# Optimization experiments

Measured on AMD Instinct MI355X. Metric: run time of the kernel, lower is better.

The kernel has to match this reference:

```python
import jax, jax.numpy as jnp
import numpy as np

HEADS = 8
DIM_HEAD = 64  # note: per-head dim is inner_dim/heads = 512 due to the module's inner_dim = dim_head*dim
SCALE = DIM_HEAD ** (-0.5)
EPS = 1e-5


def layernorm(x, gamma):
    # nn.LayerNorm(dim, elementwise_affine=False) then x * (gamma + 1)
    mu = jnp.mean(x, axis=-1, keepdims=True)
    var = jnp.var(x, axis=-1, keepdims=True)
    xn = (x - mu) * jax.lax.rsqrt(var + EPS)
    return xn * (gamma + 1.0)


def setup_inputs() -> dict:
    key = jax.random.key(0)
    ks = jax.random.split(key, 6)
    b, n, dim = 2, 2048, 256
    inner = DIM_HEAD * dim  # 4096
    x = jax.random.normal(ks[0], (b, n, dim), dtype=jnp.float32)
    gamma = jax.random.normal(ks[1], (dim,), dtype=jnp.float32) * 0.02
    Wq = jax.random.normal(ks[2], (inner, dim), dtype=jnp.float32) * 0.02
    Wk = jax.random.normal(ks[3], (inner, dim), dtype=jnp.float32) * 0.02
    Wv = jax.random.normal(ks[4], (inner, dim), dtype=jnp.float32) * 0.02
    Wo = jax.random.normal(ks[5], (dim, inner), dtype=jnp.float32) * 0.02
    return {"x": x, "gamma": gamma, "Wq": Wq, "Wk": Wk, "Wv": Wv, "Wo": Wo}


def reference(x, gamma, Wq, Wk, Wv, Wo):
    b, n, dim = x.shape
    h = HEADS
    xn = layernorm(x, gamma)  # reuse_attention=True -> norm = LayerNorm(dim)
    # self-attention: context = xn (cross_attend=False, norm_context=Identity)
    q = jnp.einsum('bnd,ed->bne', xn, Wq).reshape(b, n, h, -1).transpose(0, 2, 1, 3)
    k = jnp.einsum('bnd,ed->bne', xn, Wk).reshape(b, n, h, -1).transpose(0, 2, 1, 3)
    v = jnp.einsum('bnd,ed->bne', xn, Wv).reshape(b, n, h, -1).transpose(0, 2, 1, 3)
    qk_sim = jnp.einsum('bhqd,bhkd->bhqk', q * SCALE, k)
    attn = jax.nn.softmax(qk_sim, axis=-1)  # dropout p=0.0 -> identity
    dot = jnp.einsum('bhqk,bhkd->bhqd', attn, v)
    out = dot.transpose(0, 2, 1, 3).reshape(b, n, -1)
    out = jnp.einsum('bne,de->bnd', out, Wo)
    return out
```

## Files before the change

### kernel.cpp

```cpp
#include <hip/hip_runtime.h>


typedef unsigned short u16;
typedef unsigned int u32;
typedef __bf16 bf16x8 __attribute__((ext_vector_type(8)));
typedef float f32x4 __attribute__((ext_vector_type(4)));

__device__ __forceinline__ u16 f2bf(float f) {
    u32 u = __builtin_bit_cast(u32, f);
    u += 0x7fffu + ((u >> 16) & 1u);
    return (u16)(u >> 16);
}

#define GLDS16(G, L)                                                                  \
    __builtin_amdgcn_global_load_lds((const __attribute__((address_space(1))) u32*)(G), \
                                     (__attribute__((address_space(3))) u32*)(L), 16, 0, 0)

template <int N> __device__ __forceinline__ void vm_wait() {
    asm volatile("s_waitcnt vmcnt(%0)" :: "n"(N) : "memory");
}
__device__ __forceinline__ void lgk0() {
    asm volatile("s_waitcnt lgkmcnt(0)" ::: "memory");
}
__device__ __forceinline__ void bar() {
    __builtin_amdgcn_s_barrier();
    __builtin_amdgcn_sched_barrier(0);
}

template <typename OutT, bool ATOMIC>
__device__ __forceinline__ void gemm_core(
    const u16* __restrict__ A, const u16* __restrict__ B, OutT* __restrict__ C,
    int K, int lda, int ldb, int ldc)
{
    __shared__ u16 ldsA[3][128 * 32];
    __shared__ u16 ldsB[3][128 * 32];

    const int bm = blockIdx.y * 128;
    const int bn = blockIdx.x * 128;
    const int t = threadIdx.x;
    const int w = t >> 6, l = t & 63;
    const int wm = w >> 1, wn = w & 1;
    const int lr = l & 15, lk = l >> 4;
    const int sw = lk ^ ((lr >> 1) & 3);

    const int m0 = t >> 2, s0 = t & 3;
    const int c0 = s0 ^ ((m0 >> 1) & 3);
    const int m1 = 64 + m0;
    const int c1 = s0 ^ ((m1 >> 1) & 3);
    const int o0 = (t & ~63) * 8;
    const int o1 = (256 + (t & ~63)) * 8;

    const u16* gA0 = A + (size_t)(bm + m0) * lda + c0 * 8;
    const u16* gA1 = A + (size_t)(bm + m1) * lda + c1 * 8;
    const u16* gB0 = B + (size_t)(bn + m0) * ldb + c0 * 8;
    const u16* gB1 = B + (size_t)(bn + m1) * ldb + c1 * 8;

    f32x4 acc[4][4];
#pragma unroll
    for (int i = 0; i < 4; ++i)
#pragma unroll
        for (int j = 0; j < 4; ++j)
            acc[i][j] = f32x4{0.f, 0.f, 0.f, 0.f};

    const int nk = K >> 5;

    GLDS16(gA0, &ldsA[0][o0]); GLDS16(gA1, &ldsA[0][o1]);
    GLDS16(gB0, &ldsB[0][o0]); GLDS16(gB1, &ldsB[0][o1]);
    gA0 += 32; gA1 += 32; gB0 += 32; gB1 += 32;
    GLDS16(gA0, &ldsA[1][o0]); GLDS16(gA1, &ldsA[1][o1]);
    GLDS16(gB0, &ldsB[1][o0]); GLDS16(gB1, &ldsB[1][o1]);
    gA0 += 32; gA1 += 32; gB0 += 32; gB1 += 32;

    int cur = 0, wsl = 2;
    for (int kt = 0; kt < nk - 1; ++kt) {
        vm_wait<4>(); bar();
        if (kt + 2 < nk) {
            GLDS16(gA0, &ldsA[wsl][o0]); GLDS16(gA1, &ldsA[wsl][o1]);
            GLDS16(gB0, &ldsB[wsl][o0]); GLDS16(gB1, &ldsB[wsl][o1]);
            gA0 += 32; gA1 += 32; gB0 += 32; gB1 += 32;
        }
        bf16x8 av[4], bv[4];
#pragma unroll
        for (int i = 0; i < 4; ++i) {
            av[i] = *(const bf16x8*)&ldsA[cur][(wm * 64 + i * 16 + lr) * 32 + sw * 8];
            bv[i] = *(const bf16x8*)&ldsB[cur][(wn * 64 + i * 16 + lr) * 32 + sw * 8];
        }
        __builtin_amdgcn_s_setprio(1);
#pragma unroll
        for (int i = 0; i < 4; ++i)
#pragma unroll
            for (int j = 0; j < 4; ++j)
                acc[i][j] = __builtin_amdgcn_mfma_f32_16x16x32_bf16(av[i], bv[j], acc[i][j], 0, 0, 0);
        __builtin_amdgcn_s_setprio(0);
        cur = (cur == 2) ? 0 : cur + 1;
        wsl = (wsl == 2) ? 0 : wsl + 1;
    }
    vm_wait<0>(); bar();
    {
        bf16x8 av[4], bv[4];
#pragma unroll
        for (int i = 0; i < 4; ++i) {
            av[i] = *(const bf16x8*)&ldsA[cur][(wm * 64 + i * 16 + lr) * 32 + sw * 8];
            bv[i] = *(const bf16x8*)&ldsB[cur][(wn * 64 + i * 16 + lr) * 32 + sw * 8];
        }
        __builtin_amdgcn_s_setprio(1);
#pragma unroll
        for (int i = 0; i < 4; ++i)
#pragma unroll
            for (int j = 0; j < 4; ++j)
                acc[i][j] = __builtin_amdgcn_mfma_f32_16x16x32_bf16(av[i], bv[j], acc[i][j], 0, 0, 0);
        __builtin_amdgcn_s_setprio(0);
    }

#pragma unroll
    for (int i = 0; i < 4; ++i) {
        const int row0 = bm + wm * 64 + i * 16 + lk * 4;
#pragma unroll
        for (int j = 0; j < 4; ++j) {
            const int col = bn + wn * 64 + j * 16 + lr;
#pragma unroll
            for (int r = 0; r < 4; ++r) {
                const size_t idx = (size_t)(row0 + r) * ldc + col;
                const float v = acc[i][j][r];
                if constexpr (ATOMIC) {
                    atomicAdd(&C[idx], v);
                } else if constexpr (sizeof(OutT) == 2) {
                    C[idx] = (OutT)f2bf(v);
                } else {
                    C[idx] = (OutT)v;
                }
            }
        }
    }
}

__global__ void __launch_bounds__(256, 3) gemm_w(
    const u16* __restrict__ wkt, const u16* __restrict__ wqt,
    const u16* __restrict__ wo, const u16* __restrict__ wvt,
    float* __restrict__ MtF)
{
    const int z = blockIdx.z;
    const int zh = z & 7;
    const int q = z >> 3;
    const int which = q & 1;
    const int kc = q >> 1;
    const u16* A; const u16* B; float* C; int lda;
    if (which == 0) {
        A = wkt + (size_t)zh * 524288 + kc * 512; lda = 2048;
        B = wqt + (size_t)zh * 524288 + kc * 512;
        C = MtF + (size_t)zh * 65536;
    } else {
        A = wo + (size_t)zh * 2048 + kc * 512;    lda = 16384;
        B = wvt + (size_t)zh * 524288 + kc * 512;
        C = MtF + 524288 + (size_t)zh * 65536;
    }
    gemm_core<float, true>(A, B, C, 512, lda, 2048, 256);
}

__global__ void __launch_bounds__(256, 3) gemm_yz(
    const u16* __restrict__ xn, const u16* __restrict__ Mt,
    const u16* __restrict__ Nb, u16* __restrict__ Y, u16* __restrict__ Zt)
{
    const int z = blockIdx.z;
    const u16* A; const u16* B; u16* C;
    if (z < 2) {
        A = xn + (size_t)z * 524288;
        B = Mt;
        C = Y + (size_t)z * 4194304;
    } else {
        const int b = z - 2;
        A = Nb;
        B = xn + (size_t)b * 524288;
        C = Zt + (size_t)b * 4194304;
    }
    gemm_core<u16, false>(A, B, C, 256, 256, 256, 2048);
}

__global__ void __launch_bounds__(256) prep_kernel(
    const float* __restrict__ x, const float* __restrict__ g,
    const float* __restrict__ Wq, const float* __restrict__ Wk,
    const float* __restrict__ Wv, const float* __restrict__ Wo,
    u16* __restrict__ wqkv, u16* __restrict__ wo_b,
    u16* __restrict__ xn, float* __restrict__ MtF)
{
    __shared__ u16 tile[64][66];
    const int bid = blockIdx.x;
    const int t = threadIdx.x;
    if (bid < 3072) {
        const int bx = bid & 31, by = (bid >> 5) & 3, z = bid >> 7;
        const int wsel = z >> 3, h = z & 7;
        const float* src = (wsel == 0) ? Wq : (wsel == 1) ? Wk : Wv;
        const float scale = (wsel == 0) ? 0.125f : 1.0f;
        u16* d = wqkv + (size_t)wsel * 4194304;
        const int d0 = bx * 64;
        const int a0 = by * 64;
        const int c = t & 63, r0 = t >> 6;
#pragma unroll
        for (int rr = 0; rr < 16; ++rr) {
            const int r = r0 + rr * 4;
            tile[r][c] = f2bf(src[((size_t)h * 2048 + d0 + r) * 256 + a0 + c] * scale);
        }
        __syncthreads();
#pragma unroll
        for (int rr = 0; rr < 16; ++rr) {
            const int r = r0 + rr * 4;
            d[((size_t)h * 256 + a0 + r) * 2048 + d0 + c] = tile[c][r];
        }
    } else if (bid < 7168) {
        const size_t i = (size_t)(bid - 3072) * 256 + t;
        const float4 v = ((const float4*)Wo)[i];
        ushort4 o4;
        o4.x = f2bf(v.x); o4.y = f2bf(v.y); o4.z = f2bf(v.z); o4.w = f2bf(v.w);
        ((ushort4*)wo_b)[i] = o4;
    } else if (bid < 8192) {
        const size_t row = (size_t)(bid - 7168) * 4 + (t >> 6);
        const int l = t & 63;
        const float4 v = ((const float4*)(x + row * 256))[l];
        float s = v.x + v.y + v.z + v.w;
        float qq = v.x * v.x + v.y * v.y + v.z * v.z + v.w * v.w;
#pragma unroll
        for (int o = 32; o > 0; o >>= 1) {
            s += __shfl_xor(s, o, 64);
            qq += __shfl_xor(qq, o, 64);
        }
        const float mu = s * (1.0f / 256.0f);
        const float var = qq * (1.0f / 256.0f) - mu * mu;
        const float rs = rsqrtf(var + 1e-5f);
        const float4 gg = ((const float4*)g)[l];
        ushort4 o4;
        o4.x = f2bf((v.x - mu) * rs * (gg.x + 1.0f));
        o4.y = f2bf((v.y - mu) * rs * (gg.y + 1.0f));
        o4.z = f2bf((v.z - mu) * rs * (gg.z + 1.0f));
        o4.w = f2bf((v.w - mu) * rs * (gg.w + 1.0f));
        ((ushort4*)(xn + row * 256))[l] = o4;
    } else {
        const size_t i = (size_t)(bid - 8192) * 256 + t;
        ((float4*)MtF)[i] = float4{0.f, 0.f, 0.f, 0.f};
    }
}

__global__ void __launch_bounds__(256, 2) attn_fused(
    const u16* __restrict__ Y, const u16* __restrict__ xn,
    const u16* __restrict__ Zt, float* __restrict__ opart)
{
    __shared__ u16 ldsB[3][128 * 32];
    __shared__ u16 ldsZ[2][256 * 32];
    __shared__ u16 Pl[64 * 136];
    __shared__ float l_lds[64];

    const int wgid = blockIdx.x + 32 * blockIdx.y;
    const int xcd = wgid & 7;
    const int p = wgid >> 3;
    const int hb = 2 * xcd + (p & 1);
    const int i0 = (p >> 1) * 64;
    const int h = hb >> 1, b = hb & 1;

    const int t = threadIdx.x;
    const int w = t >> 6, l = t & 63;
    const int wm = w >> 1, wn = w & 1;
    const int lr = l & 15, lk = l >> 4;
    const int sw = lk ^ ((lr >> 1) & 3);

    if (t < 64) l_lds[t] = 0.f;

    const u16* Yb = Y + (size_t)(b * 2048 + i0) * 2048 + h * 256;
    const u16* xb = xn + (size_t)b * 2048 * 256;
    const u16* Zb = Zt + (size_t)b * 4194304 + (size_t)h * 524288;

    const int m0 = t >> 2, s0 = t & 3;
    const int c0 = s0 ^ ((m0 >> 1) & 3);
    const int m1 = 64 + m0;
    const int c1 = s0 ^ ((m1 >> 1) & 3);
    const int oB0 = (t & ~63) * 8;
    const int oB1 = (256 + (t & ~63)) * 8;

    const u16 *gZ0, *gZ1, *gZ2, *gZ3;
    const int oZ0 = (t & ~63) * 8;
    const int oZ1 = (256 + (t & ~63)) * 8;
    const int oZ2 = (512 + (t & ~63)) * 8;
    const int oZ3 = (768 + (t & ~63)) * 8;
    {
        const int q0 = t, q1 = 256 + t, q2 = 512 + t, q3 = 768 + t;
        const int mz0 = q0 >> 2, mz1 = q1 >> 2, mz2 = q2 >> 2, mz3 = q3 >> 2;
        const int cz0 = (q0 & 3) ^ ((mz0 >> 1) & 3);
        const int cz1 = (q1 & 3) ^ ((mz1 >> 1) & 3);
        const int cz2 = (q2 & 3) ^ ((mz2 >> 1) & 3);
        const int cz3 = (q3 & 3) ^ ((mz3 >> 1) & 3);
        gZ0 = Zb + (size_t)mz0 * 2048 + cz0 * 8;
        gZ1 = Zb + (size_t)mz1 * 2048 + cz1 * 8;
        gZ2 = Zb + (size_t)mz2 * 2048 + cz2 * 8;
        gZ3 = Zb + (size_t)mz3 * 2048 + cz3 * 8;
    }

    u16* ldsY = &ldsZ[0][0];
#pragma unroll
    for (int pp = 0; pp < 8; ++pp) {
        const int q = pp * 256 + t;
        const int kt = q >> 8, qq = q & 255;
        const int m = qq >> 2, s = qq & 3;
        const int c = s ^ ((m >> 1) & 3);
        GLDS16(Yb + (size_t)m * 2048 + kt * 32 + c * 8,
               &ldsY[(pp * 256 + (t & ~63)) * 8]);
    }
    GLDS16(xb + (size_t)m0 * 256 + c0 * 8, &ldsB[0][oB0]);
    GLDS16(xb + (size_t)m1 * 256 + c1 * 8, &ldsB[0][oB1]);
    GLDS16(xb + (size_t)m0 * 256 + 32 + c0 * 8, &ldsB[1][oB0]);
    GLDS16(xb + (size_t)m1 * 256 + 32 + c1 * 8, &ldsB[1][oB1]);
    vm_wait<4>();
    bar();

    bf16x8 yr[8][2];
#pragma unroll
    for (int kt = 0; kt < 8; ++kt)
#pragma unroll
        for (int i = 0; i < 2; ++i)
            yr[kt][i] = *(const bf16x8*)&ldsY[kt * 2048 + (wm * 32 + i * 16 + lr) * 32 + sw * 8];

    f32x4 acc_o[2][8];
#pragma unroll
    for (int i = 0; i < 2; ++i)
#pragma unroll
        for (int j = 0; j < 8; ++j)
            acc_o[i][j] = f32x4{0.f, 0.f, 0.f, 0.f};
    float lsum[8];
#pragma unroll
    for (int i = 0; i < 8; ++i) lsum[i] = 0.f;

#define S_STEP(KT, VMC, ISSUE)                                                        \
    {                                                                                 \
        vm_wait<VMC>(); bar();                                                        \
        ISSUE;                                                                        \
        bf16x8 bv[4];                                                                 \
        _Pragma("unroll")                                                             \
        for (int j = 0; j < 4; ++j)                                                   \
            bv[j] = *(const bf16x8*)&ldsB[(KT) % 3][(wn * 64 + j * 16 + lr) * 32 + sw * 8]; \
        __builtin_amdgcn_s_setprio(1);                                                \
        _Pragma("unroll")                                                             \
        for (int j = 0; j < 4; ++j) {                                                 \
            acc_s[0][j] = __builtin_amdgcn_mfma_f32_16x16x32_bf16(yr[KT][0], bv[j], acc_s[0][j], 0, 0, 0); \
            acc_s[1][j] = __builtin_amdgcn_mfma_f32_16x16x32_bf16(yr[KT][1], bv[j], acc_s[1][j], 0, 0, 0); \
        }                                                                             \
        __builtin_amdgcn_s_setprio(0);                                                \
    }

#define PV_STEP(KT, VMC, ISSUE)                                                       \
    {                                                                                 \
        vm_wait<VMC>(); bar();                                                        \
        ISSUE;                                                                        \
        bf16x8 av[2];                                                                 \
        av[0] = *(const bf16x8*)&Pl[(wm * 32 + lr) * 136 + (KT) * 32 + lk * 8];       \
        av[1] = *(const bf16x8*)&Pl[(wm * 32 + 16 + lr) * 136 + (KT) * 32 + lk * 8];  \
        __builtin_amdgcn_s_setprio(1);                                                \
        _Pragma("unroll")                                                             \
        for (int jf = 0; jf < 8; ++jf) {                                              \
            const bf16x8 bz = *(const bf16x8*)&ldsZ[(KT) & 1][(wn * 128 + jf * 16 + lr) * 32 + sw * 8]; \
            acc_o[0][jf] = __builtin_amdgcn_mfma_f32_16x16x32_bf16(av[0], bz, acc_o[0][jf], 0, 0, 0);   \
            acc_o[1][jf] = __builtin_amdgcn_mfma_f32_16x16x32_bf16(av[1], bz, acc_o[1][jf], 0, 0, 0);   \
        }                                                                             \
        __builtin_amdgcn_s_setprio(0);                                                \
    }

#define ISSUE_B(JBASE, KK, SLOT)                                                      \
    GLDS16(JBASE + (size_t)m0 * 256 + (KK) * 32 + c0 * 8, &ldsB[SLOT][oB0]);          \
    GLDS16(JBASE + (size_t)m1 * 256 + (KK) * 32 + c1 * 8, &ldsB[SLOT][oB1])

#define ISSUE_Z(OFF, ZBUF)                                                            \
    GLDS16(gZ0 + (OFF), &ldsZ[ZBUF][oZ0]);                                            \
    GLDS16(gZ1 + (OFF), &ldsZ[ZBUF][oZ1]);                                            \
    GLDS16(gZ2 + (OFF), &ldsZ[ZBUF][oZ2]);                                            \
    GLDS16(gZ3 + (OFF), &ldsZ[ZBUF][oZ3])

    for (int jt = 0; jt < 16; ++jt) {
        const int j0 = jt * 128;
        const int jn = ((jt + 1) & 15) * 128;
        const u16* xbj = xb + (size_t)j0 * 256;
        const u16* xbn = xb + (size_t)jn * 256;

        f32x4 acc_s[2][4];
#pragma unroll
        for (int i = 0; i < 2; ++i)
#pragma unroll
            for (int j = 0; j < 4; ++j)
                acc_s[i][j] = f32x4{0.f, 0.f, 0.f, 0.f};

        S_STEP(0, 2, ISSUE_B(xbj, 2, 2))
        S_STEP(1, 2, ISSUE_B(xbj, 3, 0))
        S_STEP(2, 2, ISSUE_B(xbj, 4, 1))
        S_STEP(3, 2, ISSUE_B(xbj, 5, 2))
        S_STEP(4, 2, ISSUE_B(xbj, 6, 0))
        S_STEP(5, 2, ISSUE_B(xbj, 7, 1))
        S_STEP(6, 2, ISSUE_Z(j0, 0))
        S_STEP(7, 4, ISSUE_Z(j0 + 32, 1))

#pragma unroll
        for (int i = 0; i < 2; ++i)
#pragma unroll
            for (int j = 0; j < 4; ++j)
#pragma unroll
                for (int r = 0; r < 4; ++r) {
                    const float e = __expf(acc_s[i][j][r]);
                    lsum[i * 4 + r] += e;
                    Pl[(wm * 32 + i * 16 + lk * 4 + r) * 136 + wn * 64 + j * 16 + lr] = f2bf(e);
                }
        lgk0();

        PV_STEP(0, 4, ((void)0))
        PV_STEP(1, 0, ISSUE_Z(j0 + 64, 0))
        PV_STEP(2, 0, ISSUE_Z(j0 + 96, 1); ISSUE_B(xbn, 0, 0))
        PV_STEP(3, 2, ISSUE_B(xbn, 1, 1))
    }

#pragma unroll
    for (int i = 0; i < 2; ++i)
#pragma unroll
        for (int r = 0; r < 4; ++r) {
            float s = lsum[i * 4 + r];
            s += __shfl_xor(s, 1, 64);
            s += __shfl_xor(s, 2, 64);
            s += __shfl_xor(s, 4, 64);
            s += __shfl_xor(s, 8, 64);
            if (lr == 0) atomicAdd(&l_lds[wm * 32 + i * 16 + lk * 4 + r], s);
        }
    __syncthreads();

    float* oh = opart + (size_t)h * 1048576;
#pragma unroll
    for (int i = 0; i < 2; ++i)
#pragma unroll
        for (int r = 0; r < 4; ++r) {
            const int row = wm * 32 + i * 16 + lk * 4 + r;
            const float rl = 1.0f / l_lds[row];
            float* orow = oh + (size_t)(b * 2048 + i0 + row) * 256 + wn * 128;
#pragma unroll
            for (int jf = 0; jf < 8; ++jf)
                orow[jf * 16 + lr] = acc_o[i][jf][r] * rl;
        }
}

__global__ void __launch_bounds__(256) hreduce_kernel(const float* __restrict__ opart,
                                                      float* __restrict__ out)
{
    const size_t i = (size_t)blockIdx.x * 256 + threadIdx.x;
    float4 s = ((const float4*)opart)[i];
#pragma unroll
    for (int h = 1; h < 8; ++h) {
        const float4 v = ((const float4*)(opart + (size_t)h * 1048576))[i];
        s.x += v.x; s.y += v.y; s.z += v.z; s.w += v.w;
    }
    ((float4*)out)[i] = s;
}

__global__ void __launch_bounds__(256) cast_bf16_kernel(const float* __restrict__ src,
                                                        u16* __restrict__ dst, float scale)
{
    const size_t i = (size_t)blockIdx.x * 256 + threadIdx.x;
    const float4 v = ((const float4*)src)[i];
    ushort4 o4;
    o4.x = f2bf(v.x * scale);
    o4.y = f2bf(v.y * scale);
    o4.z = f2bf(v.z * scale);
    o4.w = f2bf(v.w * scale);
    ((ushort4*)dst)[i] = o4;
}

extern "C" void kernel_launch(void* const* d_in, const int* in_sizes, int n_in,
                              void* d_out, int out_size, void* d_ws, size_t ws_size,
                              hipStream_t stream)
{
    (void)in_sizes; (void)n_in; (void)ws_size; (void)out_size;
    const float* x     = (const float*)d_in[0];
    const float* gamma = (const float*)d_in[1];
    const float* Wq    = (const float*)d_in[2];
    const float* Wk    = (const float*)d_in[3];
    const float* Wv    = (const float*)d_in[4];
    const float* Wo    = (const float*)d_in[5];
    float* out = (float*)d_out;

    char* ws = (char*)d_ws;
    const size_t MB = 1048576;
    u16* wqt   = (u16*)(ws);
    u16* wkt   = (u16*)(ws + 8 * MB);
    u16* wvt   = (u16*)(ws + 16 * MB);
    u16* wo    = (u16*)(ws + 24 * MB);
    u16* xn    = (u16*)(ws + 32 * MB);
    u16* Mt    = (u16*)(ws + 34 * MB);
    float* MtF = (float*)(ws + 36 * MB);
    u16* Nb    = (u16*)(ws + 35 * MB);
    u16* Y     = (u16*)(ws + 44 * MB);
    u16* Zt    = (u16*)(ws + 60 * MB);
    float* opart = (float*)(ws);

    prep_kernel<<<9216, 256, 0, stream>>>(x, gamma, Wq, Wk, Wv, Wo, wqt, wo, xn, MtF);

    gemm_w<<<dim3(2, 2, 64), 256, 0, stream>>>(wkt, wqt, wo, wvt, MtF);

    cast_bf16_kernel<<<1024, 256, 0, stream>>>(MtF, Mt, 1.0f);

    gemm_yz<<<dim3(16, 16, 4), 256, 0, stream>>>(xn, Mt, Nb, Y, Zt);

    attn_fused<<<dim3(32, 16), 256, 0, stream>>>(Y, xn, Zt, opart);

    hreduce_kernel<<<1024, 256, 0, stream>>>(opart, out);
}
```

Measured before the change: 253.8 us.

## Drop split-K atomics in weight GEMM and write bf16 output directly

The weight-product GEMM no longer splits K into four chunks with fp32 atomic accumulation. Each block now runs the full K=2048 reduction and writes bf16 results directly. This removes the MtF zeroing in prep, the atomics, and the separate cast kernel, saving two launches' worth of traffic. In exchange the grid shrinks from 256 to 64 blocks, each doing four times the work, so fewer CUs are kept busy.

```diff
diff --git a/kernel.cpp b/kernel.cpp
--- a/kernel.cpp
+++ b/kernel.cpp
@@ -137,24 +137,22 @@
 __global__ void __launch_bounds__(256, 3) gemm_w(
     const u16* __restrict__ wkt, const u16* __restrict__ wqt,
     const u16* __restrict__ wo, const u16* __restrict__ wvt,
-    float* __restrict__ MtF)
+    u16* __restrict__ Mt)
 {
     const int z = blockIdx.z;
-    const int zh = z & 7;
-    const int q = z >> 3;
-    const int which = q & 1;
-    const int kc = q >> 1;
-    const u16* A; const u16* B; float* C; int lda;
+    const int zh = z >> 1;
+    const int which = z & 1;
+    const u16* A; const u16* B; u16* C; int lda;
     if (which == 0) {
-        A = wkt + (size_t)zh * 524288 + kc * 512; lda = 2048;
-        B = wqt + (size_t)zh * 524288 + kc * 512;
-        C = MtF + (size_t)zh * 65536;
+        A = wkt + (size_t)zh * 524288; lda = 2048;
+        B = wqt + (size_t)zh * 524288;
+        C = Mt + (size_t)zh * 65536;
     } else {
-        A = wo + (size_t)zh * 2048 + kc * 512;    lda = 16384;
-        B = wvt + (size_t)zh * 524288 + kc * 512;
-        C = MtF + 524288 + (size_t)zh * 65536;
-    }
-    gemm_core<float, true>(A, B, C, 512, lda, 2048, 256);
+        A = wo + (size_t)zh * 2048;    lda = 16384;
+        B = wvt + (size_t)zh * 524288;
+        C = Mt + 524288 + (size_t)zh * 65536;
+    }
+    gemm_core<u16, false>(A, B, C, 2048, lda, 2048, 256);
 }
 
 __global__ void __launch_bounds__(256, 3) gemm_yz(
@@ -181,7 +179,7 @@
     const float* __restrict__ Wq, const float* __restrict__ Wk,
     const float* __restrict__ Wv, const float* __restrict__ Wo,
     u16* __restrict__ wqkv, u16* __restrict__ wo_b,
-    u16* __restrict__ xn, float* __restrict__ MtF)
+    u16* __restrict__ xn)
 {
     __shared__ u16 tile[64][66];
     const int bid = blockIdx.x;
@@ -212,7 +210,7 @@
         ushort4 o4;
         o4.x = f2bf(v.x); o4.y = f2bf(v.y); o4.z = f2bf(v.z); o4.w = f2bf(v.w);
         ((ushort4*)wo_b)[i] = o4;
-    } else if (bid < 8192) {
+    } else {
         const size_t row = (size_t)(bid - 7168) * 4 + (t >> 6);
         const int l = t & 63;
         const float4 v = ((const float4*)(x + row * 256))[l];
@@ -233,9 +231,6 @@
         o4.z = f2bf((v.z - mu) * rs * (gg.z + 1.0f));
         o4.w = f2bf((v.w - mu) * rs * (gg.w + 1.0f));
         ((ushort4*)(xn + row * 256))[l] = o4;
-    } else {
-        const size_t i = (size_t)(bid - 8192) * 256 + t;
-        ((float4*)MtF)[i] = float4{0.f, 0.f, 0.f, 0.f};
     }
 }
 
@@ -450,19 +445,6 @@
     ((float4*)out)[i] = s;
 }
 
-__global__ void __launch_bounds__(256) cast_bf16_kernel(const float* __restrict__ src,
-                                                        u16* __restrict__ dst, float scale)
-{
-    const size_t i = (size_t)blockIdx.x * 256 + threadIdx.x;
-    const float4 v = ((const float4*)src)[i];
-    ushort4 o4;
-    o4.x = f2bf(v.x * scale);
-    o4.y = f2bf(v.y * scale);
-    o4.z = f2bf(v.z * scale);
-    o4.w = f2bf(v.w * scale);
-    ((ushort4*)dst)[i] = o4;
-}
-
 extern "C" void kernel_launch(void* const* d_in, const int* in_sizes, int n_in,
                               void* d_out, int out_size, void* d_ws, size_t ws_size,
                               hipStream_t stream)
@@ -484,17 +466,14 @@
     u16* wo    = (u16*)(ws + 24 * MB);
     u16* xn    = (u16*)(ws + 32 * MB);
     u16* Mt    = (u16*)(ws + 34 * MB);
-    float* MtF = (float*)(ws + 36 * MB);
     u16* Nb    = (u16*)(ws + 35 * MB);
     u16* Y     = (u16*)(ws + 44 * MB);
     u16* Zt    = (u16*)(ws + 60 * MB);
     float* opart = (float*)(ws);
 
-    prep_kernel<<<9216, 256, 0, stream>>>(x, gamma, Wq, Wk, Wv, Wo, wqt, wo, xn, MtF);
-
-    gemm_w<<<dim3(2, 2, 64), 256, 0, stream>>>(wkt, wqt, wo, wvt, MtF);
-
-    cast_bf16_kernel<<<1024, 256, 0, stream>>>(MtF, Mt, 1.0f);
+    prep_kernel<<<8192, 256, 0, stream>>>(x, gamma, Wq, Wk, Wv, Wo, wqt, wo, xn);
+
+    gemm_w<<<dim3(2, 2, 16), 256, 0, stream>>>(wkt, wqt, wo, wvt, Mt);
 
     gemm_yz<<<dim3(16, 16, 4), 256, 0, stream>>>(xn, Mt, Nb, Y, Zt);
 
```

After: 262.8 us. 3.5% more time.

## Give each wave private LDS staging buffers to remove block barriers in attention loop

Applied to the files above, without the earlier changes.

Reorganizes attn_fused's shared memory so each wave loads its own slice of the xn (B) and Zt tiles into wave-private LDS regions, so the S and PV steps only need s_waitcnt rather than block-wide barriers. The P tile is moved to an XOR-swizzled layout without padding, and the prefetch schedule is reworked with sched_barrier fences. Each wave now fetches its own B/Z data, which can duplicate loads across waves (e.g. B shared by wm pairs), and two barriers per tile remain around the P exchange.

```diff
diff --git a/kernel.cpp b/kernel.cpp
--- a/kernel.cpp
+++ b/kernel.cpp
@@ -243,10 +243,7 @@
     const u16* __restrict__ Y, const u16* __restrict__ xn,
     const u16* __restrict__ Zt, float* __restrict__ opart)
 {
-    __shared__ u16 ldsB[3][128 * 32];
-    __shared__ u16 ldsZ[2][256 * 32];
-    __shared__ u16 Pl[64 * 136];
-    __shared__ float l_lds[64];
+    __shared__ u16 S_lds[40960];
 
     const int wgid = blockIdx.x + 32 * blockIdx.y;
     const int xcd = wgid & 7;
@@ -261,38 +258,31 @@
     const int lr = l & 15, lk = l >> 4;
     const int sw = lk ^ ((lr >> 1) & 3);
 
-    if (t < 64) l_lds[t] = 0.f;
+    u16* Zp  = S_lds + w * 4096;
+    u16* Pl  = S_lds + 16384;
+    u16* Bp0 = S_lds + 24576 + w * 4096;
+    u16* Bp1 = Bp0 + 2048;
 
     const u16* Yb = Y + (size_t)(b * 2048 + i0) * 2048 + h * 256;
     const u16* xb = xn + (size_t)b * 2048 * 256;
-    const u16* Zb = Zt + (size_t)b * 4194304 + (size_t)h * 524288;
-
-    const int m0 = t >> 2, s0 = t & 3;
-    const int c0 = s0 ^ ((m0 >> 1) & 3);
-    const int m1 = 64 + m0;
-    const int c1 = s0 ^ ((m1 >> 1) & 3);
-    const int oB0 = (t & ~63) * 8;
-    const int oB1 = (256 + (t & ~63)) * 8;
-
-    const u16 *gZ0, *gZ1, *gZ2, *gZ3;
-    const int oZ0 = (t & ~63) * 8;
-    const int oZ1 = (256 + (t & ~63)) * 8;
-    const int oZ2 = (512 + (t & ~63)) * 8;
-    const int oZ3 = (768 + (t & ~63)) * 8;
-    {
-        const int q0 = t, q1 = 256 + t, q2 = 512 + t, q3 = 768 + t;
-        const int mz0 = q0 >> 2, mz1 = q1 >> 2, mz2 = q2 >> 2, mz3 = q3 >> 2;
-        const int cz0 = (q0 & 3) ^ ((mz0 >> 1) & 3);
-        const int cz1 = (q1 & 3) ^ ((mz1 >> 1) & 3);
-        const int cz2 = (q2 & 3) ^ ((mz2 >> 1) & 3);
-        const int cz3 = (q3 & 3) ^ ((mz3 >> 1) & 3);
-        gZ0 = Zb + (size_t)mz0 * 2048 + cz0 * 8;
-        gZ1 = Zb + (size_t)mz1 * 2048 + cz1 * 8;
-        gZ2 = Zb + (size_t)mz2 * 2048 + cz2 * 8;
-        gZ3 = Zb + (size_t)mz3 * 2048 + cz3 * 8;
-    }
-
-    u16* ldsY = &ldsZ[0][0];
+    const u16* Zb = Zt + (size_t)b * 4194304 + (size_t)h * 524288
+                      + (size_t)(wn * 128) * 2048;
+
+    const int rq = l >> 2;
+    const int cq = (l & 3) ^ ((l >> 3) & 3);
+
+#define ISSUE_BP(JBASE, KK, DST)                                                      \
+    { _Pragma("unroll")                                                               \
+      for (int q = 0; q < 4; ++q)                                                     \
+          GLDS16(JBASE + (size_t)(wn * 64 + q * 16 + rq) * 256 + (KK) * 32 + cq * 8,  \
+                 (DST) + q * 512); }
+
+#define ISSUE_ZP(J0, KK)                                                              \
+    { _Pragma("unroll")                                                               \
+      for (int q = 0; q < 8; ++q)                                                     \
+          GLDS16(Zb + (size_t)(q * 16 + rq) * 2048 + (J0) + (KK) * 32 + cq * 8,       \
+                 Zp + q * 512); }
+
 #pragma unroll
     for (int pp = 0; pp < 8; ++pp) {
         const int q = pp * 256 + t;
@@ -300,13 +290,11 @@
         const int m = qq >> 2, s = qq & 3;
         const int c = s ^ ((m >> 1) & 3);
         GLDS16(Yb + (size_t)m * 2048 + kt * 32 + c * 8,
-               &ldsY[(pp * 256 + (t & ~63)) * 8]);
-    }
-    GLDS16(xb + (size_t)m0 * 256 + c0 * 8, &ldsB[0][oB0]);
-    GLDS16(xb + (size_t)m1 * 256 + c1 * 8, &ldsB[0][oB1]);
-    GLDS16(xb + (size_t)m0 * 256 + 32 + c0 * 8, &ldsB[1][oB0]);
-    GLDS16(xb + (size_t)m1 * 256 + 32 + c1 * 8, &ldsB[1][oB1]);
-    vm_wait<4>();
+               &S_lds[(pp * 256 + (t & ~63)) * 8]);
+    }
+    ISSUE_BP(xb, 0, Bp0);
+    ISSUE_BP(xb, 1, Bp1);
+    vm_wait<8>();
     bar();
 
     bf16x8 yr[8][2];
@@ -314,7 +302,9 @@
     for (int kt = 0; kt < 8; ++kt)
 #pragma unroll
         for (int i = 0; i < 2; ++i)
-            yr[kt][i] = *(const bf16x8*)&ldsY[kt * 2048 + (wm * 32 + i * 16 + lr) * 32 + sw * 8];
+            yr[kt][i] = *(const bf16x8*)&S_lds[kt * 2048 + (wm * 32 + i * 16 + lr) * 32 + sw * 8];
+    lgk0();
+    bar();
 
     f32x4 acc_o[2][8];
 #pragma unroll
@@ -326,14 +316,17 @@
 #pragma unroll
     for (int i = 0; i < 8; ++i) lsum[i] = 0.f;
 
-#define S_STEP(KT, VMC, ISSUE)                                                        \
+#define S_STEP(KT, ISSUE)                                                             \
     {                                                                                 \
-        vm_wait<VMC>(); bar();                                                        \
-        ISSUE;                                                                        \
+        vm_wait<4>();                                                                 \
         bf16x8 bv[4];                                                                 \
+        u16* bp = ((KT) & 1) ? Bp1 : Bp0;                                             \
         _Pragma("unroll")                                                             \
         for (int j = 0; j < 4; ++j)                                                   \
-            bv[j] = *(const bf16x8*)&ldsB[(KT) % 3][(wn * 64 + j * 16 + lr) * 32 + sw * 8]; \
+            bv[j] = *(const bf16x8*)&bp[(j * 16 + lr) * 32 + sw * 8];                 \
+        lgk0();                                                                       \
+        __builtin_amdgcn_sched_barrier(0);                                            \
+        ISSUE;                                                                        \
         __builtin_amdgcn_s_setprio(1);                                                \
         _Pragma("unroll")                                                             \
         for (int j = 0; j < 4; ++j) {                                                 \
@@ -343,38 +336,32 @@
         __builtin_amdgcn_s_setprio(0);                                                \
     }
 
-#define PV_STEP(KT, VMC, ISSUE)                                                       \
+#define PV_STEP(KT, ISSUE)                                                            \
     {                                                                                 \
-        vm_wait<VMC>(); bar();                                                        \
+        vm_wait<0>();                                                                 \
+        const int swz = (lr & 7) * 8;                                                 \
+        bf16x8 av0 = *(const bf16x8*)&Pl[(wm * 32 + lr) * 128 + (((KT) * 32 + lk * 8) ^ swz)];      \
+        bf16x8 av1 = *(const bf16x8*)&Pl[(wm * 32 + 16 + lr) * 128 + (((KT) * 32 + lk * 8) ^ swz)]; \
+        bf16x8 bz[8];                                                                 \
+        _Pragma("unroll")                                                             \
+        for (int jf = 0; jf < 8; ++jf)                                                \
+            bz[jf] = *(const bf16x8*)&Zp[(jf * 16 + lr) * 32 + sw * 8];               \
+        lgk0();                                                                       \
+        __builtin_amdgcn_sched_barrier(0);                                            \
         ISSUE;                                                                        \
-        bf16x8 av[2];                                                                 \
-        av[0] = *(const bf16x8*)&Pl[(wm * 32 + lr) * 136 + (KT) * 32 + lk * 8];       \
-        av[1] = *(const bf16x8*)&Pl[(wm * 32 + 16 + lr) * 136 + (KT) * 32 + lk * 8];  \
         __builtin_amdgcn_s_setprio(1);                                                \
         _Pragma("unroll")                                                             \
         for (int jf = 0; jf < 8; ++jf) {                                              \
-            const bf16x8 bz = *(const bf16x8*)&ldsZ[(KT) & 1][(wn * 128 + jf * 16 + lr) * 32 + sw * 8]; \
-            acc_o[0][jf] = __builtin_amdgcn_mfma_f32_16x16x32_bf16(av[0], bz, acc_o[0][jf], 0, 0, 0);   \
-            acc_o[1][jf] = __builtin_amdgcn_mfma_f32_16x16x32_bf16(av[1], bz, acc_o[1][jf], 0, 0, 0);   \
+            acc_o[0][jf] = __builtin_amdgcn_mfma_f32_16x16x32_bf16(av0, bz[jf], acc_o[0][jf], 0, 0, 0); \
+            acc_o[1][jf] = __builtin_amdgcn_mfma_f32_16x16x32_bf16(av1, bz[jf], acc_o[1][jf], 0, 0, 0); \
         }                                                                             \
         __builtin_amdgcn_s_setprio(0);                                                \
     }
 
-#define ISSUE_B(JBASE, KK, SLOT)                                                      \
-    GLDS16(JBASE + (size_t)m0 * 256 + (KK) * 32 + c0 * 8, &ldsB[SLOT][oB0]);          \
-    GLDS16(JBASE + (size_t)m1 * 256 + (KK) * 32 + c1 * 8, &ldsB[SLOT][oB1])
-
-#define ISSUE_Z(OFF, ZBUF)                                                            \
-    GLDS16(gZ0 + (OFF), &ldsZ[ZBUF][oZ0]);                                            \
-    GLDS16(gZ1 + (OFF), &ldsZ[ZBUF][oZ1]);                                            \
-    GLDS16(gZ2 + (OFF), &ldsZ[ZBUF][oZ2]);                                            \
-    GLDS16(gZ3 + (OFF), &ldsZ[ZBUF][oZ3])
-
     for (int jt = 0; jt < 16; ++jt) {
         const int j0 = jt * 128;
-        const int jn = ((jt + 1) & 15) * 128;
         const u16* xbj = xb + (size_t)j0 * 256;
-        const u16* xbn = xb + (size_t)jn * 256;
+        const u16* xbn = xb + (size_t)(((jt + 1) & 15) * 128) * 256;
 
         f32x4 acc_s[2][4];
 #pragma unroll
@@ -383,14 +370,14 @@
             for (int j = 0; j < 4; ++j)
                 acc_s[i][j] = f32x4{0.f, 0.f, 0.f, 0.f};
 
-        S_STEP(0, 2, ISSUE_B(xbj, 2, 2))
-        S_STEP(1, 2, ISSUE_B(xbj, 3, 0))
-        S_STEP(2, 2, ISSUE_B(xbj, 4, 1))
-        S_STEP(3, 2, ISSUE_B(xbj, 5, 2))
-        S_STEP(4, 2, ISSUE_B(xbj, 6, 0))
-        S_STEP(5, 2, ISSUE_B(xbj, 7, 1))
-        S_STEP(6, 2, ISSUE_Z(j0, 0))
-        S_STEP(7, 4, ISSUE_Z(j0 + 32, 1))
+        S_STEP(0, ISSUE_BP(xbj, 2, Bp0))
+        S_STEP(1, ISSUE_BP(xbj, 3, Bp1))
+        S_STEP(2, ISSUE_BP(xbj, 4, Bp0))
+        S_STEP(3, ISSUE_BP(xbj, 5, Bp1))
+        S_STEP(4, ISSUE_BP(xbj, 6, Bp0))
+        S_STEP(5, ISSUE_BP(xbj, 7, Bp1))
+        S_STEP(6, ISSUE_BP(xbn, 0, Bp0))
+        S_STEP(7, ISSUE_BP(xbn, 1, Bp1); ISSUE_ZP(j0, 0))
 
 #pragma unroll
         for (int i = 0; i < 2; ++i)
@@ -398,18 +385,26 @@
             for (int j = 0; j < 4; ++j)
 #pragma unroll
                 for (int r = 0; r < 4; ++r) {
+                    const int row = wm * 32 + i * 16 + lk * 4 + r;
+                    const int col = wn * 64 + j * 16 + lr;
                     const float e = __expf(acc_s[i][j][r]);
                     lsum[i * 4 + r] += e;
-                    Pl[(wm * 32 + i * 16 + lk * 4 + r) * 136 + wn * 64 + j * 16 + lr] = f2bf(e);
+                    Pl[row * 128 + (col ^ ((row & 7) * 8))] = f2bf(e);
                 }
         lgk0();
-
-        PV_STEP(0, 4, ((void)0))
-        PV_STEP(1, 0, ISSUE_Z(j0 + 64, 0))
-        PV_STEP(2, 0, ISSUE_Z(j0 + 96, 1); ISSUE_B(xbn, 0, 0))
-        PV_STEP(3, 2, ISSUE_B(xbn, 1, 1))
-    }
-
+        bar();
+
+        PV_STEP(0, ISSUE_ZP(j0, 1))
+        PV_STEP(1, ISSUE_ZP(j0, 2))
+        PV_STEP(2, ISSUE_ZP(j0, 3))
+        PV_STEP(3, ((void)0))
+        bar();
+    }
+
+    bar();
+    float* l_lds = (float*)Pl;
+    if (t < 64) l_lds[t] = 0.f;
+    __syncthreads();
 #pragma unroll
     for (int i = 0; i < 2; ++i)
 #pragma unroll
@@ -484,8 +479,8 @@
     u16* wo    = (u16*)(ws + 24 * MB);
     u16* xn    = (u16*)(ws + 32 * MB);
     u16* Mt    = (u16*)(ws + 34 * MB);
+    u16* Nb    = (u16*)(ws + 35 * MB);
     float* MtF = (float*)(ws + 36 * MB);
-    u16* Nb    = (u16*)(ws + 35 * MB);
     u16* Y     = (u16*)(ws + 44 * MB);
     u16* Zt    = (u16*)(ws + 60 * MB);
     float* opart = (float*)(ws);
```

After: 263.6 us. 3.9% more time.

## Restructure attention LDS pipeline, swizzle P buffer, and double M-tiles per gemm_yz block

Applied to the files above, without the earlier changes.

The attention kernel's S-phase now loads two K-slices per stage into a 2-slot, double-width B buffer, so there are half as many barriers. The P tile drops its padded stride in favour of an XOR swizzle, and the row-sum scratch now reuses the P buffer's LDS. Separately, each gemm_yz block computes two M tiles one after the other, which halves the grid and amortises setup. The trade-off is a full vmcnt(0) wait at every S stage, which lowers prefetch depth and may expose load latency.

```diff
diff --git a/kernel.cpp b/kernel.cpp
--- a/kernel.cpp
+++ b/kernel.cpp
@@ -30,13 +30,9 @@
 template <typename OutT, bool ATOMIC>
 __device__ __forceinline__ void gemm_core(
     const u16* __restrict__ A, const u16* __restrict__ B, OutT* __restrict__ C,
-    int K, int lda, int ldb, int ldc)
-{
-    __shared__ u16 ldsA[3][128 * 32];
-    __shared__ u16 ldsB[3][128 * 32];
-
-    const int bm = blockIdx.y * 128;
-    const int bn = blockIdx.x * 128;
+    int K, int lda, int ldb, int ldc, int bm, int bn,
+    u16* __restrict__ ldsA, u16* __restrict__ ldsB)
+{
     const int t = threadIdx.x;
     const int w = t >> 6, l = t & 63;
     const int wm = w >> 1, wn = w & 1;
@@ -64,26 +60,26 @@
 
     const int nk = K >> 5;
 
-    GLDS16(gA0, &ldsA[0][o0]); GLDS16(gA1, &ldsA[0][o1]);
-    GLDS16(gB0, &ldsB[0][o0]); GLDS16(gB1, &ldsB[0][o1]);
+    GLDS16(gA0, ldsA + o0); GLDS16(gA1, ldsA + o1);
+    GLDS16(gB0, ldsB + o0); GLDS16(gB1, ldsB + o1);
     gA0 += 32; gA1 += 32; gB0 += 32; gB1 += 32;
-    GLDS16(gA0, &ldsA[1][o0]); GLDS16(gA1, &ldsA[1][o1]);
-    GLDS16(gB0, &ldsB[1][o0]); GLDS16(gB1, &ldsB[1][o1]);
+    GLDS16(gA0, ldsA + 4096 + o0); GLDS16(gA1, ldsA + 4096 + o1);
+    GLDS16(gB0, ldsB + 4096 + o0); GLDS16(gB1, ldsB + 4096 + o1);
     gA0 += 32; gA1 += 32; gB0 += 32; gB1 += 32;
 
     int cur = 0, wsl = 2;
     for (int kt = 0; kt < nk - 1; ++kt) {
         vm_wait<4>(); bar();
         if (kt + 2 < nk) {
-            GLDS16(gA0, &ldsA[wsl][o0]); GLDS16(gA1, &ldsA[wsl][o1]);
-            GLDS16(gB0, &ldsB[wsl][o0]); GLDS16(gB1, &ldsB[wsl][o1]);
+            GLDS16(gA0, ldsA + wsl * 4096 + o0); GLDS16(gA1, ldsA + wsl * 4096 + o1);
+            GLDS16(gB0, ldsB + wsl * 4096 + o0); GLDS16(gB1, ldsB + wsl * 4096 + o1);
             gA0 += 32; gA1 += 32; gB0 += 32; gB1 += 32;
         }
         bf16x8 av[4], bv[4];
 #pragma unroll
         for (int i = 0; i < 4; ++i) {
-            av[i] = *(const bf16x8*)&ldsA[cur][(wm * 64 + i * 16 + lr) * 32 + sw * 8];
-            bv[i] = *(const bf16x8*)&ldsB[cur][(wn * 64 + i * 16 + lr) * 32 + sw * 8];
+            av[i] = *(const bf16x8*)&ldsA[cur * 4096 + (wm * 64 + i * 16 + lr) * 32 + sw * 8];
+            bv[i] = *(const bf16x8*)&ldsB[cur * 4096 + (wn * 64 + i * 16 + lr) * 32 + sw * 8];
         }
         __builtin_amdgcn_s_setprio(1);
 #pragma unroll
@@ -100,8 +96,8 @@
         bf16x8 av[4], bv[4];
 #pragma unroll
         for (int i = 0; i < 4; ++i) {
-            av[i] = *(const bf16x8*)&ldsA[cur][(wm * 64 + i * 16 + lr) * 32 + sw * 8];
-            bv[i] = *(const bf16x8*)&ldsB[cur][(wn * 64 + i * 16 + lr) * 32 + sw * 8];
+            av[i] = *(const bf16x8*)&ldsA[cur * 4096 + (wm * 64 + i * 16 + lr) * 32 + sw * 8];
+            bv[i] = *(const bf16x8*)&ldsB[cur * 4096 + (wn * 64 + i * 16 + lr) * 32 + sw * 8];
         }
         __builtin_amdgcn_s_setprio(1);
 #pragma unroll
@@ -139,6 +135,8 @@
     const u16* __restrict__ wo, const u16* __restrict__ wvt,
     float* __restrict__ MtF)
 {
+    __shared__ u16 ldsA[3][4096];
+    __shared__ u16 ldsB[3][4096];
     const int z = blockIdx.z;
     const int zh = z & 7;
     const int q = z >> 3;
@@ -154,13 +152,17 @@
         B = wvt + (size_t)zh * 524288 + kc * 512;
         C = MtF + 524288 + (size_t)zh * 65536;
     }
-    gemm_core<float, true>(A, B, C, 512, lda, 2048, 256);
+    gemm_core<float, true>(A, B, C, 512, lda, 2048, 256,
+                           blockIdx.y * 128, blockIdx.x * 128,
+                           &ldsA[0][0], &ldsB[0][0]);
 }
 
 __global__ void __launch_bounds__(256, 3) gemm_yz(
     const u16* __restrict__ xn, const u16* __restrict__ Mt,
     const u16* __restrict__ Nb, u16* __restrict__ Y, u16* __restrict__ Zt)
 {
+    __shared__ u16 ldsA[3][4096];
+    __shared__ u16 ldsB[3][4096];
     const int z = blockIdx.z;
     const u16* A; const u16* B; u16* C;
     if (z < 2) {
@@ -173,7 +175,13 @@
         B = xn + (size_t)b * 524288;
         C = Zt + (size_t)b * 4194304;
     }
-    gemm_core<u16, false>(A, B, C, 256, 256, 256, 2048);
+#pragma unroll
+    for (int my = 0; my < 2; ++my) {
+        gemm_core<u16, false>(A, B, C, 256, 256, 256, 2048,
+                              (blockIdx.y + 8 * my) * 128, blockIdx.x * 128,
+                              &ldsA[0][0], &ldsB[0][0]);
+        if (my == 0) { vm_wait<0>(); bar(); }
+    }
 }
 
 __global__ void __launch_bounds__(256) prep_kernel(
@@ -243,10 +251,9 @@
     const u16* __restrict__ Y, const u16* __restrict__ xn,
     const u16* __restrict__ Zt, float* __restrict__ opart)
 {
-    __shared__ u16 ldsB[3][128 * 32];
-    __shared__ u16 ldsZ[2][256 * 32];
-    __shared__ u16 Pl[64 * 136];
-    __shared__ float l_lds[64];
+    __shared__ u16 ldsB[2][8192];
+    __shared__ u16 ldsZ[2][8192];
+    __shared__ u16 Pl[8192];
 
     const int wgid = blockIdx.x + 32 * blockIdx.y;
     const int xcd = wgid & 7;
@@ -260,8 +267,6 @@
     const int wm = w >> 1, wn = w & 1;
     const int lr = l & 15, lk = l >> 4;
     const int sw = lk ^ ((lr >> 1) & 3);
-
-    if (t < 64) l_lds[t] = 0.f;
 
     const u16* Yb = Y + (size_t)(b * 2048 + i0) * 2048 + h * 256;
     const u16* xb = xn + (size_t)b * 2048 * 256;
@@ -292,6 +297,19 @@
         gZ3 = Zb + (size_t)mz3 * 2048 + cz3 * 8;
     }
 
+#define ISSUE_B_HALF(JBASE, KK, SLOT, SUB)                                            \
+    GLDS16(JBASE + (size_t)m0 * 256 + (KK) * 32 + c0 * 8, &ldsB[SLOT][(SUB) * 4096 + oB0]); \
+    GLDS16(JBASE + (size_t)m1 * 256 + (KK) * 32 + c1 * 8, &ldsB[SLOT][(SUB) * 4096 + oB1])
+
+#define ISSUE_B2(JBASE, K0, K1, SLOT)                                                 \
+    ISSUE_B_HALF(JBASE, K0, SLOT, 0); ISSUE_B_HALF(JBASE, K1, SLOT, 1)
+
+#define ISSUE_Z(OFF, ZBUF)                                                            \
+    GLDS16(gZ0 + (OFF), &ldsZ[ZBUF][oZ0]);                                            \
+    GLDS16(gZ1 + (OFF), &ldsZ[ZBUF][oZ1]);                                            \
+    GLDS16(gZ2 + (OFF), &ldsZ[ZBUF][oZ2]);                                            \
+    GLDS16(gZ3 + (OFF), &ldsZ[ZBUF][oZ3])
+
     u16* ldsY = &ldsZ[0][0];
 #pragma unroll
     for (int pp = 0; pp < 8; ++pp) {
@@ -302,10 +320,7 @@
         GLDS16(Yb + (size_t)m * 2048 + kt * 32 + c * 8,
                &ldsY[(pp * 256 + (t & ~63)) * 8]);
     }
-    GLDS16(xb + (size_t)m0 * 256 + c0 * 8, &ldsB[0][oB0]);
-    GLDS16(xb + (size_t)m1 * 256 + c1 * 8, &ldsB[0][oB1]);
-    GLDS16(xb + (size_t)m0 * 256 + 32 + c0 * 8, &ldsB[1][oB0]);
-    GLDS16(xb + (size_t)m1 * 256 + 32 + c1 * 8, &ldsB[1][oB1]);
+    ISSUE_B2(xb, 0, 1, 0);
     vm_wait<4>();
     bar();
 
@@ -315,6 +330,8 @@
 #pragma unroll
         for (int i = 0; i < 2; ++i)
             yr[kt][i] = *(const bf16x8*)&ldsY[kt * 2048 + (wm * 32 + i * 16 + lr) * 32 + sw * 8];
+    lgk0();
+    bar();
 
     f32x4 acc_o[2][8];
 #pragma unroll
@@ -326,55 +343,59 @@
 #pragma unroll
     for (int i = 0; i < 8; ++i) lsum[i] = 0.f;
 
-#define S_STEP(KT, VMC, ISSUE)                                                        \
+#define S_STEP2(KT0, KT1, SLOT, ISSUE)                                                \
     {                                                                                 \
-        vm_wait<VMC>(); bar();                                                        \
+        vm_wait<0>(); bar();                                                          \
         ISSUE;                                                                        \
-        bf16x8 bv[4];                                                                 \
-        _Pragma("unroll")                                                             \
-        for (int j = 0; j < 4; ++j)                                                   \
-            bv[j] = *(const bf16x8*)&ldsB[(KT) % 3][(wn * 64 + j * 16 + lr) * 32 + sw * 8]; \
-        __builtin_amdgcn_s_setprio(1);                                                \
-        _Pragma("unroll")                                                             \
-        for (int j = 0; j < 4; ++j) {                                                 \
-            acc_s[0][j] = __builtin_amdgcn_mfma_f32_16x16x32_bf16(yr[KT][0], bv[j], acc_s[0][j], 0, 0, 0); \
-            acc_s[1][j] = __builtin_amdgcn_mfma_f32_16x16x32_bf16(yr[KT][1], bv[j], acc_s[1][j], 0, 0, 0); \
+        {                                                                             \
+            bf16x8 bv[4];                                                             \
+            _Pragma("unroll")                                                         \
+            for (int j = 0; j < 4; ++j)                                               \
+                bv[j] = *(const bf16x8*)&ldsB[SLOT][(wn * 64 + j * 16 + lr) * 32 + sw * 8]; \
+            __builtin_amdgcn_s_setprio(1);                                            \
+            _Pragma("unroll")                                                         \
+            for (int j = 0; j < 4; ++j) {                                             \
+                acc_s[0][j] = __builtin_amdgcn_mfma_f32_16x16x32_bf16(yr[KT0][0], bv[j], acc_s[0][j], 0, 0, 0); \
+                acc_s[1][j] = __builtin_amdgcn_mfma_f32_16x16x32_bf16(yr[KT0][1], bv[j], acc_s[1][j], 0, 0, 0); \
+            }                                                                         \
+            __builtin_amdgcn_s_setprio(0);                                            \
         }                                                                             \
-        __builtin_amdgcn_s_setprio(0);                                                \
+        {                                                                             \
+            bf16x8 bv[4];                                                             \
+            _Pragma("unroll")                                                         \
+            for (int j = 0; j < 4; ++j)                                               \
+                bv[j] = *(const bf16x8*)&ldsB[SLOT][4096 + (wn * 64 + j * 16 + lr) * 32 + sw * 8]; \
+            __builtin_amdgcn_s_setprio(1);                                            \
+            _Pragma("unroll")                                                         \
+            for (int j = 0; j < 4; ++j) {                                             \
+                acc_s[0][j] = __builtin_amdgcn_mfma_f32_16x16x32_bf16(yr[KT1][0], bv[j], acc_s[0][j], 0, 0, 0); \
+                acc_s[1][j] = __builtin_amdgcn_mfma_f32_16x16x32_bf16(yr[KT1][1], bv[j], acc_s[1][j], 0, 0, 0); \
+            }                                                                         \
+            __builtin_amdgcn_s_setprio(0);                                            \
+        }                                                                             \
     }
 
 #define PV_STEP(KT, VMC, ISSUE)                                                       \
     {                                                                                 \
         vm_wait<VMC>(); bar();                                                        \
         ISSUE;                                                                        \
-        bf16x8 av[2];                                                                 \
-        av[0] = *(const bf16x8*)&Pl[(wm * 32 + lr) * 136 + (KT) * 32 + lk * 8];       \
-        av[1] = *(const bf16x8*)&Pl[(wm * 32 + 16 + lr) * 136 + (KT) * 32 + lk * 8];  \
+        const int swz = (lr & 7) * 8;                                                 \
+        bf16x8 av0 = *(const bf16x8*)&Pl[(wm * 32 + lr) * 128 + (((KT) * 32 + lk * 8) ^ swz)];      \
+        bf16x8 av1 = *(const bf16x8*)&Pl[(wm * 32 + 16 + lr) * 128 + (((KT) * 32 + lk * 8) ^ swz)]; \
         __builtin_amdgcn_s_setprio(1);                                                \
         _Pragma("unroll")                                                             \
         for (int jf = 0; jf < 8; ++jf) {                                              \
             const bf16x8 bz = *(const bf16x8*)&ldsZ[(KT) & 1][(wn * 128 + jf * 16 + lr) * 32 + sw * 8]; \
-            acc_o[0][jf] = __builtin_amdgcn_mfma_f32_16x16x32_bf16(av[0], bz, acc_o[0][jf], 0, 0, 0);   \
-            acc_o[1][jf] = __builtin_amdgcn_mfma_f32_16x16x32_bf16(av[1], bz, acc_o[1][jf], 0, 0, 0);   \
+            acc_o[0][jf] = __builtin_amdgcn_mfma_f32_16x16x32_bf16(av0, bz, acc_o[0][jf], 0, 0, 0);   \
+            acc_o[1][jf] = __builtin_amdgcn_mfma_f32_16x16x32_bf16(av1, bz, acc_o[1][jf], 0, 0, 0);   \
         }                                                                             \
         __builtin_amdgcn_s_setprio(0);                                                \
     }
 
-#define ISSUE_B(JBASE, KK, SLOT)                                                      \
-    GLDS16(JBASE + (size_t)m0 * 256 + (KK) * 32 + c0 * 8, &ldsB[SLOT][oB0]);          \
-    GLDS16(JBASE + (size_t)m1 * 256 + (KK) * 32 + c1 * 8, &ldsB[SLOT][oB1])
-
-#define ISSUE_Z(OFF, ZBUF)                                                            \
-    GLDS16(gZ0 + (OFF), &ldsZ[ZBUF][oZ0]);                                            \
-    GLDS16(gZ1 + (OFF), &ldsZ[ZBUF][oZ1]);                                            \
-    GLDS16(gZ2 + (OFF), &ldsZ[ZBUF][oZ2]);                                            \
-    GLDS16(gZ3 + (OFF), &ldsZ[ZBUF][oZ3])
-
     for (int jt = 0; jt < 16; ++jt) {
         const int j0 = jt * 128;
-        const int jn = ((jt + 1) & 15) * 128;
         const u16* xbj = xb + (size_t)j0 * 256;
-        const u16* xbn = xb + (size_t)jn * 256;
+        const u16* xbn = xb + (size_t)(((jt + 1) & 15) * 128) * 256;
 
         f32x4 acc_s[2][4];
 #pragma unroll
@@ -383,14 +404,11 @@
             for (int j = 0; j < 4; ++j)
                 acc_s[i][j] = f32x4{0.f, 0.f, 0.f, 0.f};
 
-        S_STEP(0, 2, ISSUE_B(xbj, 2, 2))
-        S_STEP(1, 2, ISSUE_B(xbj, 3, 0))
-        S_STEP(2, 2, ISSUE_B(xbj, 4, 1))
-        S_STEP(3, 2, ISSUE_B(xbj, 5, 2))
-        S_STEP(4, 2, ISSUE_B(xbj, 6, 0))
-        S_STEP(5, 2, ISSUE_B(xbj, 7, 1))
-        S_STEP(6, 2, ISSUE_Z(j0, 0))
-        S_STEP(7, 4, ISSUE_Z(j0 + 32, 1))
+        S_STEP2(0, 1, 0, ISSUE_B2(xbj, 2, 3, 1))
+        S_STEP2(2, 3, 1, ISSUE_B2(xbj, 4, 5, 0))
+        S_STEP2(4, 5, 0, ISSUE_B2(xbj, 6, 7, 1))
+        S_STEP2(6, 7, 1, ISSUE_Z(j0, 0))
+        ISSUE_Z(j0 + 32, 1);
 
 #pragma unroll
         for (int i = 0; i < 2; ++i)
@@ -398,18 +416,24 @@
             for (int j = 0; j < 4; ++j)
 #pragma unroll
                 for (int r = 0; r < 4; ++r) {
+                    const int row = wm * 32 + i * 16 + lk * 4 + r;
+                    const int col = wn * 64 + j * 16 + lr;
                     const float e = __expf(acc_s[i][j][r]);
                     lsum[i * 4 + r] += e;
-                    Pl[(wm * 32 + i * 16 + lk * 4 + r) * 136 + wn * 64 + j * 16 + lr] = f2bf(e);
+                    Pl[row * 128 + (col ^ ((row & 7) * 8))] = f2bf(e);
                 }
         lgk0();
 
         PV_STEP(0, 4, ((void)0))
         PV_STEP(1, 0, ISSUE_Z(j0 + 64, 0))
-        PV_STEP(2, 0, ISSUE_Z(j0 + 96, 1); ISSUE_B(xbn, 0, 0))
-        PV_STEP(3, 2, ISSUE_B(xbn, 1, 1))
-    }
-
+        PV_STEP(2, 0, ISSUE_Z(j0 + 96, 1); ISSUE_B_HALF(xbn, 0, 0, 0))
+        PV_STEP(3, 2, ISSUE_B_HALF(xbn, 1, 0, 1))
+    }
+
+    bar();
+    float* l_lds = (float*)Pl;
+    if (t < 64) l_lds[t] = 0.f;
+    __syncthreads();
 #pragma unroll
     for (int i = 0; i < 2; ++i)
 #pragma unroll
@@ -484,8 +508,8 @@
     u16* wo    = (u16*)(ws + 24 * MB);
     u16* xn    = (u16*)(ws + 32 * MB);
     u16* Mt    = (u16*)(ws + 34 * MB);
+    u16* Nb    = (u16*)(ws + 35 * MB);
     float* MtF = (float*)(ws + 36 * MB);
-    u16* Nb    = (u16*)(ws + 35 * MB);
     u16* Y     = (u16*)(ws + 44 * MB);
     u16* Zt    = (u16*)(ws + 60 * MB);
     float* opart = (float*)(ws);
@@ -496,7 +520,7 @@
 
     cast_bf16_kernel<<<1024, 256, 0, stream>>>(MtF, Mt, 1.0f);
 
-    gemm_yz<<<dim3(16, 16, 4), 256, 0, stream>>>(xn, Mt, Nb, Y, Zt);
+    gemm_yz<<<dim3(16, 8, 4), 256, 0, stream>>>(xn, Mt, Nb, Y, Zt);
 
     attn_fused<<<dim3(32, 16), 256, 0, stream>>>(Y, xn, Zt, opart);
 
```

After: 254.0 us. No clear change (+0.1%).
